# Performance work log

Measured on AMD Instinct MI355X. Metric: run time of the kernel, lower is better.

## Reference

```python
import jax, jax.numpy as jnp
import numpy as np

B, S, D = 8, 1024, 512


def setup_inputs() -> dict:
    key = jax.random.key(0)
    k1, k2, k3, k4, k5, k6, k7 = jax.random.split(key, 7)
    inp = jax.random.normal(k1, (B, S, D), dtype=jnp.float32)
    aspect = jax.random.normal(k2, (B, S, D), dtype=jnp.float32)
    # lengths in [S//2, S], with max exactly S (the module requires max(len)==S)
    inp_len = jax.random.randint(k3, (B,), S // 2, S + 1).astype(jnp.float32)
    inp_len = inp_len.at[0].set(float(S))
    lim = float(np.sqrt(6.0 / (D + D)))  # xavier_uniform bound
    w1 = jax.random.uniform(k4, (D, D), jnp.float32, -lim, lim)
    b1 = jax.random.uniform(k5, (D,), jnp.float32, -lim, lim)
    w2 = jax.random.uniform(k6, (D, D), jnp.float32, -lim, lim)
    b2 = jax.random.uniform(k7, (D,), jnp.float32, -lim, lim)
    return {"inp": inp, "inp_len": inp_len, "aspect": aspect,
            "w1": w1, "b1": b1, "w2": w2, "b2": b2}


def reference(inp, inp_len, aspect, w1, b1, w2, b2):
    # inp, aspect: [B,S,D]; inp_len: [B] float lengths with max == S
    Bv, Sv, Dv = inp.shape
    scale = jnp.sqrt(inp_len)[:, None, None]                      # [B,1,1]
    att = jnp.einsum('bsd,btd->bst', aspect, inp) / scale          # [B,S,S]
    # mask over the query (row) dimension, as in the original expand
    mask = (jnp.arange(Sv)[None, :] < inp_len.astype(jnp.int32)[:, None]).astype(inp.dtype)  # [B,S]
    exp = att * mask[:, :, None]
    att_n = exp / (jnp.sum(exp, axis=-1, keepdims=True) + 1e-4)    # linear (non-exp) normalize
    weighted = jnp.einsum('bst,btd->bsd', att_n, inp)              # [B,S,D]
    ffn_inp = weighted + (inp + aspect) * mask[:, :, None]
    # FFN: two square linears with relu, plus inner residual
    o1 = jax.nn.relu(jnp.einsum('bsd,ed->bse', ffn_inp, w1) + b1)
    o2 = jax.nn.relu(jnp.einsum('bsd,ed->bse', o1, w2) + b2)
    ffn_out = o2 + ffn_inp
    final = ffn_inp + ffn_out
    return final / jnp.linalg.norm(final, axis=2, keepdims=True)
```

## Files before the change

kernel.cpp:

```cpp
#include <hip/hip_runtime.h>

#define Bq 8
#define Sq 1024
#define Dq 512

typedef __attribute__((ext_vector_type(8))) short bf16x8;
typedef __attribute__((ext_vector_type(4))) float f32x4;

__device__ __forceinline__ unsigned short f2bf(float f) {
  unsigned int u = __float_as_uint(f);
  return (unsigned short)((u + 0x7fffu + ((u >> 16) & 1u)) >> 16);
}

__device__ __forceinline__ void load_lds16(const unsigned short* g, unsigned short* l) {
  __builtin_amdgcn_global_load_lds(
      (const __attribute__((address_space(1))) unsigned int*)g,
      (__attribute__((address_space(3))) unsigned int*)l, 16, 0, 0);
}


__global__ __launch_bounds__(256) void prep_t(
    const float* __restrict__ inp,
    unsigned short* __restrict__ inpT, float* __restrict__ partial) {
  __shared__ unsigned short tile[64][66];
  __shared__ float csum[16][64];
  int idx = blockIdx.x;
  int tid = threadIdx.x;
  int b = idx & 7, tt = (idx >> 3) & 15, dd = idx >> 7;
  int r = tid >> 4, c4 = (tid & 15) * 4;
  const float* src = inp + ((size_t)b * Sq + tt * 64) * Dq + dd * 64;
  float cp0 = 0.f, cp1 = 0.f, cp2 = 0.f, cp3 = 0.f;
#pragma unroll
  for (int p = 0; p < 4; ++p) {
    float4 v = *(const float4*)(src + (size_t)(r + p * 16) * Dq + c4);
    ushort4 o; o.x = f2bf(v.x); o.y = f2bf(v.y); o.z = f2bf(v.z); o.w = f2bf(v.w);
    *(ushort4*)&tile[r + p * 16][c4] = o;
    cp0 += v.x; cp1 += v.y; cp2 += v.z; cp3 += v.w;
  }
  csum[r][c4] = cp0; csum[r][c4 + 1] = cp1; csum[r][c4 + 2] = cp2; csum[r][c4 + 3] = cp3;
  __syncthreads();
  unsigned short* dst = inpT + (size_t)b * Dq * Sq + (size_t)dd * 64 * Sq + tt * 64;
#pragma unroll
  for (int p = 0; p < 4; ++p) {
    int d = (tid >> 4) + p * 16;
    int tq = (tid & 15) * 4;
    ushort4 o;
    o.x = tile[tq][d]; o.y = tile[tq + 1][d]; o.z = tile[tq + 2][d]; o.w = tile[tq + 3][d];
    *(ushort4*)(dst + (size_t)d * Sq + tq) = o;
  }
  if (tid < 64) {
    float s = 0.f;
#pragma unroll
    for (int rr = 0; rr < 16; ++rr) s += csum[rr][tid];
    partial[((size_t)b * 16 + tt) * Dq + dd * 64 + tid] = s;
  }
}

__global__ __launch_bounds__(256, 5) void gram_fac(
    const unsigned short* __restrict__ inpT, const float* __restrict__ partial,
    const float* __restrict__ aspect, const float* __restrict__ lenv,
    const float* __restrict__ w1, const float* __restrict__ w2,
    unsigned short* __restrict__ Gm, float* __restrict__ fac,
    unsigned short* __restrict__ asp_bf,
    unsigned short* __restrict__ w1b, unsigned short* __restrict__ w2b) {
  __shared__ unsigned short sA[2][32 * 64];
  __shared__ unsigned short sB[2][64 * 64];
  int idx = blockIdx.x;
  int tid = threadIdx.x;
  int lane = tid & 63, wave = tid >> 6;

  if (idx >= 2048) {
    int blk = idx - 2048;
    const float* src = (blk < 256) ? w1 : w2;
    unsigned short* dst = (blk < 256) ? w1b : w2b;
    int li = ((blk & 255) * 256 + tid) * 4;
    int n = li >> 9, k = li & 511;
    float4 v = *(const float4*)(src + li);
    ushort4 o; o.x = f2bf(v.x); o.y = f2bf(v.y); o.z = f2bf(v.z); o.w = f2bf(v.w);
    int x = ((k >> 3) & 3) ^ ((n >> 1) & 3);
    int off = (k >> 5) * 16384 + n * 32 + x * 8 + (k & 7);
    *(ushort4*)(dst + off) = o;
    return;
  }
  if (idx >= 1536) {
    int blk = idx - 1536;
    const float* s = aspect + (size_t)blk * 8192 + tid * 4;
    unsigned short* d = asp_bf + (size_t)blk * 8192 + tid * 4;
#pragma unroll
    for (int j = 0; j < 8; ++j) {
      float4 v = *(const float4*)(s + j * 1024);
      ushort4 o; o.x = f2bf(v.x); o.y = f2bf(v.y); o.z = f2bf(v.z); o.w = f2bf(v.w);
      *(ushort4*)(d + j * 1024) = o;
    }
    return;
  }
  if (idx >= 1024) {
    float* cs = (float*)sA;
    int fblk = idx - 1024;
    int b = fblk >> 6;
    int s0 = (fblk & 63) * 16;
#pragma unroll
    for (int h = 0; h < 2; ++h) {
      int d = h * 256 + tid;
      float s = 0.f;
      const float* p = partial + (size_t)b * 16 * Dq + d;
#pragma unroll
      for (int t = 0; t < 16; ++t) s += p[t * Dq];
      cs[d] = s;
    }
    __syncthreads();
    int g = lane >> 4, lr = lane & 15;
    int row = s0 + wave * 4 + g;
    const float* a = aspect + ((size_t)b * Sq + row) * Dq + lr * 32;
    float sum = 0.f;
#pragma unroll
    for (int j = 0; j < 8; ++j) {
      float4 v = *(const float4*)(a + j * 4);
      const float* c = cs + lr * 32 + j * 4;
      sum += v.x * c[0] + v.y * c[1] + v.z * c[2] + v.w * c[3];
    }
#pragma unroll
    for (int off = 1; off < 16; off <<= 1) sum += __shfl_xor(sum, off, 64);
    if (lr == 0) {
      float len = lenv[b];
      float scale = sqrtf(len);
      float f = 0.f;
      if (row < (int)len) f = 1.f / (scale * (sum / scale + 1e-4f));
      fac[b * Sq + row] = f;
    }
    return;
  }

  const int K = 1024;
  int b = idx & 7;
  int tile = idx >> 3;
  int bm = tile & 15, bn = tile >> 4;
  const unsigned short* Ab = inpT + (size_t)b * Dq * Sq + (size_t)bm * 32 * K;
  const unsigned short* Bb = inpT + (size_t)b * Dq * Sq + (size_t)bn * 64 * K;
  int lr = lane & 15, lq = lane >> 4;
  int x7 = lr & 7;
  int l3 = lane >> 3, l7 = lane & 7;

  const unsigned short* gA = Ab + (size_t)(wave * 8 + l3) * K + (l7 ^ l3) * 8;
  const unsigned short* gB = Bb + (size_t)(wave * 16 + l3) * K + (l7 ^ l3) * 8;
  int dbaseA = (wave * 64 + lane) * 8;
  int dbaseB0 = (wave * 128 + lane) * 8;
  int dbaseB1 = (wave * 128 + 64 + lane) * 8;

  f32x4 acc[2] = {};

  auto issue = [&](int buf, int k0) {
    load_lds16(gA + k0, &sA[buf][dbaseA]);
    load_lds16(gB + k0, &sB[buf][dbaseB0]);
    load_lds16(gB + (size_t)8 * K + k0, &sB[buf][dbaseB1]);
  };

  int wm = (wave & 1) * 16, wn = (wave >> 1) * 32;
  issue(0, 0);
#pragma unroll
  for (int it = 0; it < 16; ++it) {
    int cur = it & 1;
    if (it + 1 < 16) {
      issue(cur ^ 1, (it + 1) << 6);
      asm volatile("s_waitcnt vmcnt(3)" ::: "memory");
    } else {
      asm volatile("s_waitcnt vmcnt(0)" ::: "memory");
    }
    __builtin_amdgcn_s_barrier();
#pragma unroll
    for (int c = 0; c < 2; ++c) {
      int g = c * 4 + lq;
      bf16x8 a0 = *(const bf16x8*)&sA[cur][((wm + lr) * 8 + (g ^ x7)) * 8];
      bf16x8 b0 = *(const bf16x8*)&sB[cur][((wn + lr) * 8 + (g ^ x7)) * 8];
      bf16x8 b1 = *(const bf16x8*)&sB[cur][((wn + 16 + lr) * 8 + (g ^ x7)) * 8];
      acc[0] = __builtin_amdgcn_mfma_f32_16x16x32_bf16(a0, b0, acc[0], 0, 0, 0);
      acc[1] = __builtin_amdgcn_mfma_f32_16x16x32_bf16(a0, b1, acc[1], 0, 0, 0);
    }
    asm volatile("s_waitcnt lgkmcnt(0)" ::: "memory");
    __builtin_amdgcn_sched_barrier(0);
    __builtin_amdgcn_s_barrier();
  }

  unsigned short* sP = sA[0];
#pragma unroll
  for (int ni = 0; ni < 2; ++ni)
#pragma unroll
    for (int i = 0; i < 4; ++i) {
      int rl = wm + lq * 4 + i;
      int ccl = wn + ni * 16 + lr;
      int x = (rl >> 3) ^ ((ccl >> 1) & 3);
      sP[ccl * 32 + x * 8 + (rl & 7)] = f2bf(acc[ni][i]);
    }
  __syncthreads();
  unsigned short* Ob = Gm + (size_t)b * 512 * 512 + (size_t)bm * 16384 + (size_t)bn * 2048;
  *(bf16x8*)(Ob + tid * 8) = *(const bf16x8*)(sP + tid * 8);
}

#define MEGA_SMEM (16 * 512 * 2 + 2 * 16384 * 2)

__global__ __launch_bounds__(512, 4) void mega_ffn(
    const unsigned short* __restrict__ aspb, const unsigned short* __restrict__ G,
    const unsigned short* __restrict__ w1b, const unsigned short* __restrict__ w2b,
    const float* __restrict__ b1, const float* __restrict__ b2,
    const float* __restrict__ inp, const float* __restrict__ aspect,
    const float* __restrict__ fac, const float* __restrict__ lenv,
    float* __restrict__ out) {
  extern __shared__ char smem[];
  unsigned short* ldsA = (unsigned short*)smem;
  unsigned short* wbuf = (unsigned short*)(smem + 16 * 512 * 2);
  int tid = threadIdx.x;
  int lane = tid & 63, wave = tid >> 6;
  int lr = lane & 15, lq = lane >> 4;
  int xb = blockIdx.x;
  int bid = ((xb & 7) << 6) | (xb >> 3);
  int r0 = bid * 16;
  int b = bid >> 6;
  int c0 = wave * 64;

  f32x4 acc[4];
  float ffnv[4][4];

  int bx = (lq ^ ((lr >> 1) & 3)) * 8;
  int rdbase = (c0 + lr) * 32 + bx;

  auto aoff = [&](int rr, int c) {
    int cq = c >> 3;
    return rr * 512 + ((cq ^ (rr & 7)) << 3) + (c & 7);
  };

  int soff = tid * 8;
  auto stage = [&](int buf, int kc, const unsigned short* Bsrc) {
    const unsigned short* src = Bsrc + kc * 16384;
    unsigned short* dstb = wbuf + buf * 16384;
#pragma unroll
    for (int i = 0; i < 4; ++i)
      load_lds16(src + i * 4096 + soff, dstb + i * 4096 + soff);
  };

  auto gemmPhase = [&](const unsigned short* Bsrc) {
#pragma unroll
    for (int t = 0; t < 4; ++t) acc[t] = (f32x4){0.f, 0.f, 0.f, 0.f};
    stage(0, 0, Bsrc);
#pragma unroll
    for (int kc = 0; kc < 16; ++kc) {
      int cur = kc & 1;
      if (kc < 15) {
        stage(cur ^ 1, kc + 1, Bsrc);
        asm volatile("s_waitcnt vmcnt(4)" ::: "memory");
      } else {
        asm volatile("s_waitcnt vmcnt(0)" ::: "memory");
      }
      __builtin_amdgcn_s_barrier();
      bf16x8 afr = *(const bf16x8*)&ldsA[aoff(lr, kc * 32 + lq * 8)];
      bf16x8 bfr[4];
#pragma unroll
      for (int t = 0; t < 4; ++t)
        bfr[t] = *(const bf16x8*)&wbuf[cur * 16384 + rdbase + t * 512];
#pragma unroll
      for (int t = 0; t < 4; ++t)
        acc[t] = __builtin_amdgcn_mfma_f32_16x16x32_bf16(afr, bfr[t], acc[t], 0, 0, 0);
      asm volatile("s_waitcnt lgkmcnt(0)" ::: "memory");
      __builtin_amdgcn_sched_barrier(0);
      __builtin_amdgcn_s_barrier();
    }
  };

#pragma unroll
  for (int h = 0; h < 2; ++h) {
    int s = h * 512 + tid;
    int rr = s >> 6;
    int sq = s & 63;
    int cq = sq ^ (rr & 7);
    load_lds16(aspb + (size_t)(r0 + rr) * 512 + cq * 8, ldsA + s * 8);
  }

  gemmPhase(G + (size_t)b * 512 * 512);
  int len = (int)lenv[b];
  float facv[4];
#pragma unroll
  for (int i = 0; i < 4; ++i) facv[i] = fac[r0 + lq * 4 + i];
#pragma unroll
  for (int t = 0; t < 4; ++t)
#pragma unroll
    for (int i = 0; i < 4; ++i) {
      int rr = lq * 4 + i;
      int r = r0 + rr;
      size_t idx = (size_t)r * 512 + c0 + t * 16 + lr;
      float add = ((r & 1023) < len) ? (inp[idx] + aspect[idx]) : 0.f;
      float v = acc[t][i] * facv[i] + add;
      ffnv[t][i] = v;
      ldsA[aoff(rr, c0 + t * 16 + lr)] = f2bf(v);
    }
  __syncthreads();

  gemmPhase(w1b);
  float biasv[4];
#pragma unroll
  for (int t = 0; t < 4; ++t) biasv[t] = b1[c0 + t * 16 + lr];
#pragma unroll
  for (int t = 0; t < 4; ++t)
#pragma unroll
    for (int i = 0; i < 4; ++i) {
      int rr = lq * 4 + i;
      ldsA[aoff(rr, c0 + t * 16 + lr)] = f2bf(fmaxf(acc[t][i] + biasv[t], 0.f));
    }
  __syncthreads();

  gemmPhase(w2b);
#pragma unroll
  for (int t = 0; t < 4; ++t) biasv[t] = b2[c0 + t * 16 + lr];
  float ssq[4] = {0.f, 0.f, 0.f, 0.f};
#pragma unroll
  for (int t = 0; t < 4; ++t)
#pragma unroll
    for (int i = 0; i < 4; ++i) {
      float v = 2.f * ffnv[t][i] + fmaxf(acc[t][i] + biasv[t], 0.f);
      ffnv[t][i] = v;
      ssq[i] += v * v;
    }
#pragma unroll
  for (int off = 1; off < 16; off <<= 1)
#pragma unroll
    for (int i = 0; i < 4; ++i) ssq[i] += __shfl_xor(ssq[i], off, 64);
  float* ssqW = (float*)wbuf;
  if (lr == 0)
#pragma unroll
    for (int i = 0; i < 4; ++i) ssqW[wave * 16 + lq * 4 + i] = ssq[i];
  __syncthreads();
  float rn[4];
#pragma unroll
  for (int i = 0; i < 4; ++i) {
    float s = 0.f;
#pragma unroll
    for (int w = 0; w < 8; ++w) s += ssqW[w * 16 + lq * 4 + i];
    rn[i] = 1.f / sqrtf(s);
  }
#pragma unroll
  for (int t = 0; t < 4; ++t)
#pragma unroll
    for (int i = 0; i < 4; ++i) {
      int r = r0 + lq * 4 + i;
      out[(size_t)r * 512 + c0 + t * 16 + lr] = ffnv[t][i] * rn[i];
    }
}

extern "C" void kernel_launch(void* const* d_in, const int* in_sizes, int n_in,
                              void* d_out, int out_size, void* d_ws, size_t ws_size,
                              hipStream_t stream) {
  const float* inp = (const float*)d_in[0];
  const float* inp_len = (const float*)d_in[1];
  const float* aspect = (const float*)d_in[2];
  const float* w1 = (const float*)d_in[3];
  const float* b1 = (const float*)d_in[4];
  const float* w2 = (const float*)d_in[5];
  const float* b2 = (const float*)d_in[6];
  float* out = (float*)d_out;

  char* W = (char*)d_ws;
  const size_t MB = 1ull << 20;
  unsigned short* asp_bf = (unsigned short*)(W + 0);
  unsigned short* inpT   = (unsigned short*)(W + 8 * MB);
  unsigned short* Gm     = (unsigned short*)(W + 16 * MB);
  unsigned short* w1bf   = (unsigned short*)(W + 20 * MB);
  unsigned short* w2bf   = (unsigned short*)(W + 20 * MB + 512 * 1024);
  float*          partial= (float*)(W + 21 * MB);
  float*          fac    = (float*)(W + 22 * MB);

  prep_t<<<1024, 256, 0, stream>>>(inp, inpT, partial);

  gram_fac<<<2560, 256, 0, stream>>>(inpT, partial, aspect, inp_len, w1, w2,
                                     Gm, fac, asp_bf, w1bf, w2bf);

  hipFuncSetAttribute((const void*)mega_ffn,
                      hipFuncAttributeMaxDynamicSharedMemorySize, MEGA_SMEM);
  mega_ffn<<<512, 512, MEGA_SMEM, stream>>>(
      asp_bf, Gm, w1bf, w2bf, b1, b2, inp, aspect, fac, inp_len, out);
}
```

Before: 139.6 us.

## Double rows per FFN block and read weights straight from global into registers

The fused FFN kernel now handles 32 rows per block instead of 16, so the grid is halved and each weight fragment feeds two MFMAs. Weight tiles are no longer staged through LDS with barriers. Each wave loads its B fragments from global memory into a three-deep register ring and prefetches the A fragments from LDS one step ahead, with the MFMA block raised to high priority. This removes the per-k-step barriers and the LDS staging traffic. In exchange it uses more registers, allows only 2 blocks per CU, and relies on L2/cache hits for the repeated weight loads.

```diff
diff --git a/kernel.cpp b/kernel.cpp
--- a/kernel.cpp
+++ b/kernel.cpp
@@ -196,152 +196,169 @@
   *(bf16x8*)(Ob + tid * 8) = *(const bf16x8*)(sP + tid * 8);
 }
 
-#define MEGA_SMEM (16 * 512 * 2 + 2 * 16384 * 2)
-
-__global__ __launch_bounds__(512, 4) void mega_ffn(
+__global__ __launch_bounds__(512, 2) void mega_ffn(
     const unsigned short* __restrict__ aspb, const unsigned short* __restrict__ G,
     const unsigned short* __restrict__ w1b, const unsigned short* __restrict__ w2b,
     const float* __restrict__ b1, const float* __restrict__ b2,
     const float* __restrict__ inp, const float* __restrict__ aspect,
     const float* __restrict__ fac, const float* __restrict__ lenv,
     float* __restrict__ out) {
-  extern __shared__ char smem[];
-  unsigned short* ldsA = (unsigned short*)smem;
-  unsigned short* wbuf = (unsigned short*)(smem + 16 * 512 * 2);
+  __shared__ unsigned short ldsA[32 * 512];
+  __shared__ float ssqW[8 * 32];
   int tid = threadIdx.x;
   int lane = tid & 63, wave = tid >> 6;
   int lr = lane & 15, lq = lane >> 4;
-  int xb = blockIdx.x;
-  int bid = ((xb & 7) << 6) | (xb >> 3);
-  int r0 = bid * 16;
-  int b = bid >> 6;
+  int batch = blockIdx.x & 7;
+  int pos = blockIdx.x >> 3;
+  int r0 = batch * 1024 + pos * 32;
   int c0 = wave * 64;
 
-  f32x4 acc[4];
-  float ffnv[4][4];
-
-  int bx = (lq ^ ((lr >> 1) & 3)) * 8;
-  int rdbase = (c0 + lr) * 32 + bx;
+  f32x4 acc[2][4];
+  float ffnv[2][4][4];
 
   auto aoff = [&](int rr, int c) {
     int cq = c >> 3;
     return rr * 512 + ((cq ^ (rr & 7)) << 3) + (c & 7);
   };
-
-  int soff = tid * 8;
-  auto stage = [&](int buf, int kc, const unsigned short* Bsrc) {
-    const unsigned short* src = Bsrc + kc * 16384;
-    unsigned short* dstb = wbuf + buf * 16384;
-#pragma unroll
-    for (int i = 0; i < 4; ++i)
-      load_lds16(src + i * 4096 + soff, dstb + i * 4096 + soff);
+  auto baddr = [&](const unsigned short* Bp, int kc, int cc) {
+    return Bp + kc * 16384 + cc * 32 + ((lq ^ ((cc >> 1) & 3)) << 3);
   };
 
-  auto gemmPhase = [&](const unsigned short* Bsrc) {
-#pragma unroll
-    for (int t = 0; t < 4; ++t) acc[t] = (f32x4){0.f, 0.f, 0.f, 0.f};
-    stage(0, 0, Bsrc);
+  auto gemmPhase = [&](const unsigned short* Bp) {
+    bf16x8 bq[3][4];
+    bf16x8 aq[2][2];
+#pragma unroll
+    for (int m = 0; m < 2; ++m)
+#pragma unroll
+      for (int t = 0; t < 4; ++t) acc[m][t] = (f32x4){0.f, 0.f, 0.f, 0.f};
+#pragma unroll
+    for (int t = 0; t < 4; ++t) {
+      bq[0][t] = *(const bf16x8*)baddr(Bp, 0, c0 + t * 16 + lr);
+      bq[1][t] = *(const bf16x8*)baddr(Bp, 1, c0 + t * 16 + lr);
+    }
+#pragma unroll
+    for (int m = 0; m < 2; ++m)
+      aq[0][m] = *(const bf16x8*)&ldsA[aoff(m * 16 + lr, lq * 8)];
 #pragma unroll
     for (int kc = 0; kc < 16; ++kc) {
-      int cur = kc & 1;
-      if (kc < 15) {
-        stage(cur ^ 1, kc + 1, Bsrc);
-        asm volatile("s_waitcnt vmcnt(4)" ::: "memory");
-      } else {
-        asm volatile("s_waitcnt vmcnt(0)" ::: "memory");
-      }
-      __builtin_amdgcn_s_barrier();
-      bf16x8 afr = *(const bf16x8*)&ldsA[aoff(lr, kc * 32 + lq * 8)];
-      bf16x8 bfr[4];
-#pragma unroll
-      for (int t = 0; t < 4; ++t)
-        bfr[t] = *(const bf16x8*)&wbuf[cur * 16384 + rdbase + t * 512];
-#pragma unroll
-      for (int t = 0; t < 4; ++t)
-        acc[t] = __builtin_amdgcn_mfma_f32_16x16x32_bf16(afr, bfr[t], acc[t], 0, 0, 0);
-      asm volatile("s_waitcnt lgkmcnt(0)" ::: "memory");
-      __builtin_amdgcn_sched_barrier(0);
-      __builtin_amdgcn_s_barrier();
+      if (kc + 2 < 16) {
+#pragma unroll
+        for (int t = 0; t < 4; ++t)
+          bq[(kc + 2) % 3][t] = *(const bf16x8*)baddr(Bp, kc + 2, c0 + t * 16 + lr);
+      }
+      if (kc + 1 < 16) {
+#pragma unroll
+        for (int m = 0; m < 2; ++m)
+          aq[(kc + 1) & 1][m] =
+              *(const bf16x8*)&ldsA[aoff(m * 16 + lr, (kc + 1) * 32 + lq * 8)];
+      }
+      __builtin_amdgcn_s_setprio(1);
+#pragma unroll
+      for (int t = 0; t < 4; ++t) {
+        acc[0][t] = __builtin_amdgcn_mfma_f32_16x16x32_bf16(aq[kc & 1][0], bq[kc % 3][t],
+                                                            acc[0][t], 0, 0, 0);
+        acc[1][t] = __builtin_amdgcn_mfma_f32_16x16x32_bf16(aq[kc & 1][1], bq[kc % 3][t],
+                                                            acc[1][t], 0, 0, 0);
+      }
+      __builtin_amdgcn_s_setprio(0);
     }
   };
 
 #pragma unroll
-  for (int h = 0; h < 2; ++h) {
+  for (int h = 0; h < 8; ++h) {
     int s = h * 512 + tid;
-    int rr = s >> 6;
-    int sq = s & 63;
+    int rr = s >> 6, sq = s & 63;
     int cq = sq ^ (rr & 7);
     load_lds16(aspb + (size_t)(r0 + rr) * 512 + cq * 8, ldsA + s * 8);
   }
-
-  gemmPhase(G + (size_t)b * 512 * 512);
-  int len = (int)lenv[b];
-  float facv[4];
-#pragma unroll
-  for (int i = 0; i < 4; ++i) facv[i] = fac[r0 + lq * 4 + i];
-#pragma unroll
-  for (int t = 0; t < 4; ++t)
-#pragma unroll
-    for (int i = 0; i < 4; ++i) {
-      int rr = lq * 4 + i;
-      int r = r0 + rr;
-      size_t idx = (size_t)r * 512 + c0 + t * 16 + lr;
-      float add = ((r & 1023) < len) ? (inp[idx] + aspect[idx]) : 0.f;
-      float v = acc[t][i] * facv[i] + add;
-      ffnv[t][i] = v;
-      ldsA[aoff(rr, c0 + t * 16 + lr)] = f2bf(v);
-    }
+  asm volatile("s_waitcnt vmcnt(0)" ::: "memory");
+  __syncthreads();
+
+  gemmPhase(G + (size_t)batch * 512 * 512);
+  int len = (int)lenv[batch];
+  float facv[2][4];
+#pragma unroll
+  for (int m = 0; m < 2; ++m)
+#pragma unroll
+    for (int i = 0; i < 4; ++i) facv[m][i] = fac[r0 + m * 16 + lq * 4 + i];
+  __syncthreads();
+#pragma unroll
+  for (int m = 0; m < 2; ++m)
+#pragma unroll
+    for (int t = 0; t < 4; ++t)
+#pragma unroll
+      for (int i = 0; i < 4; ++i) {
+        int rr = m * 16 + lq * 4 + i;
+        int gr = r0 + rr;
+        size_t idx = (size_t)gr * 512 + c0 + t * 16 + lr;
+        float add = ((gr & 1023) < len) ? (inp[idx] + aspect[idx]) : 0.f;
+        float v = acc[m][t][i] * facv[m][i] + add;
+        ffnv[m][t][i] = v;
+        ldsA[aoff(rr, c0 + t * 16 + lr)] = f2bf(v);
+      }
   __syncthreads();
 
   gemmPhase(w1b);
   float biasv[4];
 #pragma unroll
   for (int t = 0; t < 4; ++t) biasv[t] = b1[c0 + t * 16 + lr];
-#pragma unroll
-  for (int t = 0; t < 4; ++t)
+  __syncthreads();
+#pragma unroll
+  for (int m = 0; m < 2; ++m)
+#pragma unroll
+    for (int t = 0; t < 4; ++t)
+#pragma unroll
+      for (int i = 0; i < 4; ++i) {
+        int rr = m * 16 + lq * 4 + i;
+        ldsA[aoff(rr, c0 + t * 16 + lr)] = f2bf(fmaxf(acc[m][t][i] + biasv[t], 0.f));
+      }
+  __syncthreads();
+
+  gemmPhase(w2b);
+#pragma unroll
+  for (int t = 0; t < 4; ++t) biasv[t] = b2[c0 + t * 16 + lr];
+  float ssq[2][4] = {{0.f, 0.f, 0.f, 0.f}, {0.f, 0.f, 0.f, 0.f}};
+#pragma unroll
+  for (int m = 0; m < 2; ++m)
+#pragma unroll
+    for (int t = 0; t < 4; ++t)
+#pragma unroll
+      for (int i = 0; i < 4; ++i) {
+        float v = 2.f * ffnv[m][t][i] + fmaxf(acc[m][t][i] + biasv[t], 0.f);
+        ffnv[m][t][i] = v;
+        ssq[m][i] += v * v;
+      }
+#pragma unroll
+  for (int off = 1; off < 16; off <<= 1)
+#pragma unroll
+    for (int m = 0; m < 2; ++m)
+#pragma unroll
+      for (int i = 0; i < 4; ++i) ssq[m][i] += __shfl_xor(ssq[m][i], off, 64);
+  if (lr == 0)
+#pragma unroll
+    for (int m = 0; m < 2; ++m)
+#pragma unroll
+      for (int i = 0; i < 4; ++i) ssqW[wave * 32 + m * 16 + lq * 4 + i] = ssq[m][i];
+  __syncthreads();
+  float rn[2][4];
+#pragma unroll
+  for (int m = 0; m < 2; ++m)
 #pragma unroll
     for (int i = 0; i < 4; ++i) {
-      int rr = lq * 4 + i;
-      ldsA[aoff(rr, c0 + t * 16 + lr)] = f2bf(fmaxf(acc[t][i] + biasv[t], 0.f));
-    }
-  __syncthreads();
-
-  gemmPhase(w2b);
-#pragma unroll
-  for (int t = 0; t < 4; ++t) biasv[t] = b2[c0 + t * 16 + lr];
-  float ssq[4] = {0.f, 0.f, 0.f, 0.f};
-#pragma unroll
-  for (int t = 0; t < 4; ++t)
-#pragma unroll
-    for (int i = 0; i < 4; ++i) {
-      float v = 2.f * ffnv[t][i] + fmaxf(acc[t][i] + biasv[t], 0.f);
-      ffnv[t][i] = v;
-      ssq[i] += v * v;
-    }
-#pragma unroll
-  for (int off = 1; off < 16; off <<= 1)
-#pragma unroll
-    for (int i = 0; i < 4; ++i) ssq[i] += __shfl_xor(ssq[i], off, 64);
-  float* ssqW = (float*)wbuf;
-  if (lr == 0)
-#pragma unroll
-    for (int i = 0; i < 4; ++i) ssqW[wave * 16 + lq * 4 + i] = ssq[i];
-  __syncthreads();
-  float rn[4];
-#pragma unroll
-  for (int i = 0; i < 4; ++i) {
-    float s = 0.f;
-#pragma unroll
-    for (int w = 0; w < 8; ++w) s += ssqW[w * 16 + lq * 4 + i];
-    rn[i] = 1.f / sqrtf(s);
-  }
-#pragma unroll
-  for (int t = 0; t < 4; ++t)
-#pragma unroll
-    for (int i = 0; i < 4; ++i) {
-      int r = r0 + lq * 4 + i;
-      out[(size_t)r * 512 + c0 + t * 16 + lr] = ffnv[t][i] * rn[i];
-    }
+      float s = 0.f;
+#pragma unroll
+      for (int w = 0; w < 8; ++w) s += ssqW[w * 32 + m * 16 + lq * 4 + i];
+      rn[m][i] = 1.f / sqrtf(s);
+    }
+#pragma unroll
+  for (int m = 0; m < 2; ++m)
+#pragma unroll
+    for (int t = 0; t < 4; ++t)
+#pragma unroll
+      for (int i = 0; i < 4; ++i) {
+        int gr = r0 + m * 16 + lq * 4 + i;
+        out[(size_t)gr * 512 + c0 + t * 16 + lr] = ffnv[m][t][i] * rn[m][i];
+      }
 }
 
 extern "C" void kernel_launch(void* const* d_in, const int* in_sizes, int n_in,
@@ -371,8 +388,6 @@
   gram_fac<<<2560, 256, 0, stream>>>(inpT, partial, aspect, inp_len, w1, w2,
                                      Gm, fac, asp_bf, w1bf, w2bf);
 
-  hipFuncSetAttribute((const void*)mega_ffn,
-                      hipFuncAttributeMaxDynamicSharedMemorySize, MEGA_SMEM);
-  mega_ffn<<<512, 512, MEGA_SMEM, stream>>>(
+  mega_ffn<<<256, 512, 0, stream>>>(
       asp_bf, Gm, w1bf, w2bf, b1, b2, inp, aspect, fac, inp_len, out);
 }
```

New measurement: 130.3 us. -6.6%, faster.
